# Kernel tuning notes

Measured on AMD Instinct MI355X. Metric: run time of the kernel, lower is better.

## Reference

```python
import jax, jax.numpy as jnp
import numpy as np

N = 2097152
D = 128


def setup_inputs() -> dict:
    key = jax.random.key(0)
    k1, k2, k3, k4 = jax.random.split(key, 4)
    x = jax.random.normal(k1, (N, D), dtype=jnp.float32)
    pos = jax.random.normal(k2, (N, 3), dtype=jnp.float32)
    ori = jax.random.normal(k3, (N, 3), dtype=jnp.float32)
    seq = jnp.arange(N, dtype=jnp.int64).reshape(N, 1)
    batch = jnp.sort(jax.random.randint(k4, (N,), 0, 64)).astype(jnp.int64)
    return {"x": x, "pos": pos, "seq": seq, "ori": ori, "batch": batch}


def _segment_index(seq):
    # idx = group id from consecutive runs of seq//2 (floor division)
    s = seq[:, 0] // 2
    d = jnp.concatenate([s, s[-1:]])
    change = (d[:-1] != d[1:]).astype(jnp.float32)
    idx = (jnp.cumsum(change) - change).astype(jnp.int32)
    return idx


def reference(x, pos, seq, ori, batch):
    n = x.shape[0]
    num_seg = n // 2  # exact for seq = arange(N): pairs of consecutive nodes
    idx = _segment_index(seq)

    counts = jax.ops.segment_sum(jnp.ones((n,), dtype=x.dtype), idx,
                                 num_segments=num_seg)
    denom = jnp.maximum(counts, 1.0)[:, None]

    x_out = jax.ops.segment_sum(x, idx, num_segments=num_seg) / denom
    pos_out = jax.ops.segment_sum(pos, idx, num_segments=num_seg) / denom
    seq_out = jax.ops.segment_max(seq // 2, idx, num_segments=num_seg)
    ori_mean = jax.ops.segment_sum(ori, idx, num_segments=num_seg) / denom
    # F.normalize(ori, p=2, dim=-1)
    norm = jnp.linalg.norm(ori_mean, axis=-1, keepdims=True)
    ori_out = ori_mean / jnp.maximum(norm, 1e-12)
    batch_out = jax.ops.segment_max(batch, idx, num_segments=num_seg)
    return (x_out, pos_out, seq_out, ori_out, batch_out)
```

## Files before the change

### kernel.cpp

```cpp
#include <hip/hip_runtime.h>
#include <math.h>

__global__ void x_avg_kernel(const float4* __restrict__ x,
                             float4* __restrict__ xo,
                             long total ) {
    long i = (long)blockIdx.x * blockDim.x + threadIdx.x;
    if (i >= total) return;
    long seg = i >> 5;
    long j   = i & 31;
    float4 a = x[seg * 64 + j];
    float4 b = x[seg * 64 + 32 + j];
    float4 o;
    o.x = (a.x + b.x) * 0.5f;
    o.y = (a.y + b.y) * 0.5f;
    o.z = (a.z + b.z) * 0.5f;
    o.w = (a.w + b.w) * 0.5f;
    xo[i] = o;
}

__global__ void misc_kernel(const float* __restrict__ pos,
                            const int*   __restrict__ seq,
                            const float* __restrict__ ori,
                            const int*   __restrict__ batch,
                            float* __restrict__ pos_out,
                            float* __restrict__ seq_out,
                            float* __restrict__ ori_out,
                            float* __restrict__ batch_out,
                            int S) {
    int s = blockIdx.x * blockDim.x + threadIdx.x;
    if (s >= S) return;
    long p0 = (long)(2 * s) * 3;

    float px = (pos[p0 + 0] + pos[p0 + 3]) * 0.5f;
    float py = (pos[p0 + 1] + pos[p0 + 4]) * 0.5f;
    float pz = (pos[p0 + 2] + pos[p0 + 5]) * 0.5f;
    long o3 = (long)s * 3;
    pos_out[o3 + 0] = px;
    pos_out[o3 + 1] = py;
    pos_out[o3 + 2] = pz;

    float ox = (ori[p0 + 0] + ori[p0 + 3]) * 0.5f;
    float oy = (ori[p0 + 1] + ori[p0 + 4]) * 0.5f;
    float oz = (ori[p0 + 2] + ori[p0 + 5]) * 0.5f;
    float nrm = sqrtf(ox * ox + oy * oy + oz * oz);
    float inv = 1.0f / fmaxf(nrm, 1e-12f);
    ori_out[o3 + 0] = ox * inv;
    ori_out[o3 + 1] = oy * inv;
    ori_out[o3 + 2] = oz * inv;

    int s0 = seq[2 * s]     >> 1;
    int s1 = seq[2 * s + 1] >> 1;
    seq_out[s] = (float)(s0 > s1 ? s0 : s1);

    int b0 = batch[2 * s];
    int b1 = batch[2 * s + 1];
    batch_out[s] = (float)(b0 > b1 ? b0 : b1);
}

extern "C" void kernel_launch(void* const* d_in, const int* in_sizes, int n_in,
                              void* d_out, int out_size, void* d_ws, size_t ws_size,
                              hipStream_t stream) {
    const float* x     = (const float*)d_in[0];
    const float* pos   = (const float*)d_in[1];
    const int*   seq   = (const int*)d_in[2];
    const float* ori   = (const float*)d_in[3];
    const int*   batch = (const int*)d_in[4];

    const int N = in_sizes[2];
    const int S = N / 2;

    float* out       = (float*)d_out;
    float* x_out     = out;
    float* pos_out   = out + (size_t)S * 128;
    float* seq_out   = out + (size_t)S * 131;
    float* ori_out   = out + (size_t)S * 132;
    float* batch_out = out + (size_t)S * 135;

    const long total = (long)S * 32;
    const int block = 256;
    const long grid_x = (total + block - 1) / block;
    x_avg_kernel<<<dim3((unsigned)grid_x), dim3(block), 0, stream>>>(
        (const float4*)x, (float4*)x_out, total);

    const int grid_m = (S + block - 1) / block;
    misc_kernel<<<dim3(grid_m), dim3(block), 0, stream>>>(
        pos, seq, ori, batch, pos_out, seq_out, ori_out, batch_out, S);
}
```

Measured before the change: 1.539 ms.

## Fuse pooling kernels into one grid-stride kernel with nontemporal vector I/O

Merges the x-averaging kernel and the small-field kernel into one persistent grid-stride kernel launched with a fixed 2048-block grid. It switches loads and stores to nontemporal vector builtins and processes pos/ori/seq/batch two segments per thread so every access is a 16-byte or 8-byte vector. The goal is to cut one launch, improve coalescing of the 3-float fields, and avoid cache pollution on a purely streaming workload. The fixed grid could leave bandwidth unused if it is too small to keep enough memory requests in flight. The 16-byte vector loads on pos and ori also assume those buffers are suitably aligned.

```diff
diff --git a/kernel.cpp b/kernel.cpp
--- a/kernel.cpp
+++ b/kernel.cpp
@@ -1,60 +1,114 @@
 #include <hip/hip_runtime.h>
 #include <math.h>
 
-__global__ void x_avg_kernel(const float4* __restrict__ x,
-                             float4* __restrict__ xo,
-                             long total ) {
-    long i = (long)blockIdx.x * blockDim.x + threadIdx.x;
-    if (i >= total) return;
-    long seg = i >> 5;
-    long j   = i & 31;
-    float4 a = x[seg * 64 + j];
-    float4 b = x[seg * 64 + 32 + j];
-    float4 o;
-    o.x = (a.x + b.x) * 0.5f;
-    o.y = (a.y + b.y) * 0.5f;
-    o.z = (a.z + b.z) * 0.5f;
-    o.w = (a.w + b.w) * 0.5f;
-    xo[i] = o;
-}
+typedef float f32x4 __attribute__((ext_vector_type(4)));
+typedef float f32x2 __attribute__((ext_vector_type(2)));
+typedef int   i32x4 __attribute__((ext_vector_type(4)));
 
-__global__ void misc_kernel(const float* __restrict__ pos,
-                            const int*   __restrict__ seq,
-                            const float* __restrict__ ori,
-                            const int*   __restrict__ batch,
-                            float* __restrict__ pos_out,
-                            float* __restrict__ seq_out,
-                            float* __restrict__ ori_out,
-                            float* __restrict__ batch_out,
-                            int S) {
-    int s = blockIdx.x * blockDim.x + threadIdx.x;
-    if (s >= S) return;
-    long p0 = (long)(2 * s) * 3;
+__global__ __launch_bounds__(256) void fused_pool_kernel(
+    const f32x4* __restrict__ x4,
+    f32x4*       __restrict__ xo4,
+    const float* __restrict__ pos,
+    const int*   __restrict__ seq,
+    const float* __restrict__ ori,
+    const int*   __restrict__ batch,
+    float* __restrict__ pos_out,
+    float* __restrict__ seq_out,
+    float* __restrict__ ori_out,
+    float* __restrict__ batch_out,
+    long total4, int S)
+{
+    const long nth = (long)gridDim.x * blockDim.x;
+    const long tid = (long)blockIdx.x * blockDim.x + threadIdx.x;
 
-    float px = (pos[p0 + 0] + pos[p0 + 3]) * 0.5f;
-    float py = (pos[p0 + 1] + pos[p0 + 4]) * 0.5f;
-    float pz = (pos[p0 + 2] + pos[p0 + 5]) * 0.5f;
-    long o3 = (long)s * 3;
-    pos_out[o3 + 0] = px;
-    pos_out[o3 + 1] = py;
-    pos_out[o3 + 2] = pz;
+    #pragma unroll 4
+    for (long i = tid; i < total4; i += nth) {
+        const long seg = i >> 5;
+        const long j   = i & 31;
+        const f32x4* pa = &x4[seg * 64 + j];
+        f32x4 a = __builtin_nontemporal_load(pa);
+        f32x4 b = __builtin_nontemporal_load(pa + 32);
+        f32x4 o = (a + b) * 0.5f;
+        __builtin_nontemporal_store(o, &xo4[i]);
+    }
 
-    float ox = (ori[p0 + 0] + ori[p0 + 3]) * 0.5f;
-    float oy = (ori[p0 + 1] + ori[p0 + 4]) * 0.5f;
-    float oz = (ori[p0 + 2] + ori[p0 + 5]) * 0.5f;
-    float nrm = sqrtf(ox * ox + oy * oy + oz * oz);
-    float inv = 1.0f / fmaxf(nrm, 1e-12f);
-    ori_out[o3 + 0] = ox * inv;
-    ori_out[o3 + 1] = oy * inv;
-    ori_out[o3 + 2] = oz * inv;
+    const long pairs = (long)S >> 1;
+    for (long t = tid; t < pairs; t += nth) {
+        {
+            const f32x4* p4 = (const f32x4*)(pos + 12 * t);
+            f32x4 p0 = __builtin_nontemporal_load(p4 + 0);
+            f32x4 p1 = __builtin_nontemporal_load(p4 + 1);
+            f32x4 p2 = __builtin_nontemporal_load(p4 + 2);
+            f32x2 w0, w1, w2;
+            w0.x = (p0.x + p0.w) * 0.5f;
+            w0.y = (p0.y + p1.x) * 0.5f;
+            w1.x = (p0.z + p1.y) * 0.5f;
+            w1.y = (p1.z + p2.y) * 0.5f;
+            w2.x = (p1.w + p2.z) * 0.5f;
+            w2.y = (p2.x + p2.w) * 0.5f;
+            f32x2* po2 = (f32x2*)(pos_out + 6 * t);
+            __builtin_nontemporal_store(w0, po2 + 0);
+            __builtin_nontemporal_store(w1, po2 + 1);
+            __builtin_nontemporal_store(w2, po2 + 2);
+        }
+        {
+            const f32x4* o4 = (const f32x4*)(ori + 12 * t);
+            f32x4 q0 = __builtin_nontemporal_load(o4 + 0);
+            f32x4 q1 = __builtin_nontemporal_load(o4 + 1);
+            f32x4 q2 = __builtin_nontemporal_load(o4 + 2);
+            float oax = (q0.x + q0.w) * 0.5f;
+            float oay = (q0.y + q1.x) * 0.5f;
+            float oaz = (q0.z + q1.y) * 0.5f;
+            float obx = (q1.z + q2.y) * 0.5f;
+            float oby = (q1.w + q2.z) * 0.5f;
+            float obz = (q2.x + q2.w) * 0.5f;
+            float ia = 1.0f / fmaxf(sqrtf(oax*oax + oay*oay + oaz*oaz), 1e-12f);
+            float ib = 1.0f / fmaxf(sqrtf(obx*obx + oby*oby + obz*obz), 1e-12f);
+            f32x2 w0, w1, w2;
+            w0.x = oax * ia; w0.y = oay * ia;
+            w1.x = oaz * ia; w1.y = obx * ib;
+            w2.x = oby * ib; w2.y = obz * ib;
+            f32x2* oo2 = (f32x2*)(ori_out + 6 * t);
+            __builtin_nontemporal_store(w0, oo2 + 0);
+            __builtin_nontemporal_store(w1, oo2 + 1);
+            __builtin_nontemporal_store(w2, oo2 + 2);
+        }
+        {
+            i32x4 sq = __builtin_nontemporal_load((const i32x4*)(seq + 4 * t));
+            int sa0 = sq.x >> 1, sa1 = sq.y >> 1;
+            int sb0 = sq.z >> 1, sb1 = sq.w >> 1;
+            f32x2 sw;
+            sw.x = (float)(sa0 > sa1 ? sa0 : sa1);
+            sw.y = (float)(sb0 > sb1 ? sb0 : sb1);
+            __builtin_nontemporal_store(sw, (f32x2*)(seq_out + 2 * t));
 
-    int s0 = seq[2 * s]     >> 1;
-    int s1 = seq[2 * s + 1] >> 1;
-    seq_out[s] = (float)(s0 > s1 ? s0 : s1);
+            i32x4 bq = __builtin_nontemporal_load((const i32x4*)(batch + 4 * t));
+            f32x2 bw;
+            bw.x = (float)(bq.x > bq.y ? bq.x : bq.y);
+            bw.y = (float)(bq.z > bq.w ? bq.z : bq.w);
+            __builtin_nontemporal_store(bw, (f32x2*)(batch_out + 2 * t));
+        }
+    }
 
-    int b0 = batch[2 * s];
-    int b1 = batch[2 * s + 1];
-    batch_out[s] = (float)(b0 > b1 ? b0 : b1);
+    if ((S & 1) && tid == 0) {
+        int s = S - 1;
+        long p0i = (long)(2 * s) * 3;
+        long o3  = (long)s * 3;
+        pos_out[o3 + 0] = (pos[p0i + 0] + pos[p0i + 3]) * 0.5f;
+        pos_out[o3 + 1] = (pos[p0i + 1] + pos[p0i + 4]) * 0.5f;
+        pos_out[o3 + 2] = (pos[p0i + 2] + pos[p0i + 5]) * 0.5f;
+        float ox = (ori[p0i + 0] + ori[p0i + 3]) * 0.5f;
+        float oy = (ori[p0i + 1] + ori[p0i + 4]) * 0.5f;
+        float oz = (ori[p0i + 2] + ori[p0i + 5]) * 0.5f;
+        float inv = 1.0f / fmaxf(sqrtf(ox*ox + oy*oy + oz*oz), 1e-12f);
+        ori_out[o3 + 0] = ox * inv;
+        ori_out[o3 + 1] = oy * inv;
+        ori_out[o3 + 2] = oz * inv;
+        int s0 = seq[2 * s] >> 1, s1 = seq[2 * s + 1] >> 1;
+        seq_out[s] = (float)(s0 > s1 ? s0 : s1);
+        int b0 = batch[2 * s], b1 = batch[2 * s + 1];
+        batch_out[s] = (float)(b0 > b1 ? b0 : b1);
+    }
 }
 
 extern "C" void kernel_launch(void* const* d_in, const int* in_sizes, int n_in,
@@ -76,13 +130,11 @@
     float* ori_out   = out + (size_t)S * 132;
     float* batch_out = out + (size_t)S * 135;
 
-    const long total = (long)S * 32;
+    const long total4 = (long)S * 32;
+
     const int block = 256;
-    const long grid_x = (total + block - 1) / block;
-    x_avg_kernel<<<dim3((unsigned)grid_x), dim3(block), 0, stream>>>(
-        (const float4*)x, (float4*)x_out, total);
-
-    const int grid_m = (S + block - 1) / block;
-    misc_kernel<<<dim3(grid_m), dim3(block), 0, stream>>>(
-        pos, seq, ori, batch, pos_out, seq_out, ori_out, batch_out, S);
+    const int grid  = 2048;
+    fused_pool_kernel<<<dim3(grid), dim3(block), 0, stream>>>(
+        (const f32x4*)x, (f32x4*)x_out, pos, seq, ori, batch,
+        pos_out, seq_out, ori_out, batch_out, total4, S);
 }
```

Measured after the change: 1.556 ms. About the same (+1.1%).
